# Kernel tuning notes

Measured on AMD Instinct MI355X. Metric: run time of the kernel, lower is better.

Reference implementation:

```python
import jax, jax.numpy as jnp
import numpy as np

B, U, L, H, M = 4, 16, 128, 768, 256   # docs, utterances/doc, tokens/utt, hidden, mentions/doc
HID = 150                               # Score MLP hidden dim
N_CLUSTERS = 32


def setup_inputs() -> dict:
    key = jax.random.key(0)
    ks = jax.random.split(key, 8)
    hidden = jax.random.normal(ks[0], (B, U, L, H), jnp.float32)

    rng = np.random.default_rng(0)
    span_utt = rng.integers(0, U, (B, M))
    span_start = rng.integers(0, L - 8, (B, M))
    span_end = span_start + rng.integers(1, 9, (B, M))  # span length in [1, 8]

    # coreference labels: label[i, j] = 1 iff j is a true antecedent (j < i, same cluster);
    # if mention i has no antecedent, label[i, i] = 1 (the epsilon / new-entity slot).
    clusters = rng.integers(0, N_CLUSTERS, (B, M))
    same = clusters[:, :, None] == clusters[:, None, :]
    ant = same & np.tril(np.ones((M, M), bool), -1)
    labels = ant.astype(np.float32)
    diag = np.arange(M)
    labels[:, diag, diag] = (~ant.any(-1)).astype(np.float32)

    scale = 0.02
    W1 = jax.random.normal(ks[1], (3 * H, HID), jnp.float32) * scale
    W2 = jax.random.normal(ks[2], (HID, HID), jnp.float32) * scale
    W3 = jax.random.normal(ks[3], (HID, 1), jnp.float32) * scale
    return {
        "hidden": hidden,
        "span_utt": jnp.asarray(span_utt, jnp.int32),
        "span_start": jnp.asarray(span_start, jnp.int32),
        "span_end": jnp.asarray(span_end, jnp.int32),
        "labels": jnp.asarray(labels),
        "W1": W1, "b1": jnp.zeros((HID,), jnp.float32),
        "W2": W2, "b2": jnp.zeros((HID,), jnp.float32),
        "W3": W3, "b3": jnp.zeros((1,), jnp.float32),
    }


def reference(hidden, span_utt, span_start, span_end, labels, W1, b1, W2, b2, W3, b3):
    # ---- span mean-pooling (EntityEncoder, aggr='mean') ----
    pos = jnp.arange(L)
    mask = (pos[None, None, :] >= span_start[..., None]) & (pos[None, None, :] < span_end[..., None])
    w = mask.astype(hidden.dtype) / (span_end - span_start)[..., None].astype(hidden.dtype)  # [B,M,L]
    gathered = jnp.take_along_axis(hidden, span_utt[:, :, None, None], axis=1)  # [B,M,L,H]
    pooled = jnp.einsum('bml,bmlh->bmh', w, gathered)  # [B,M,H]

    # ---- pairwise antecedent scoring (PairScorer / Score MLP, dropout=eval) ----
    ii, jj = np.tril_indices(M, -1)  # static pair indices, P = M(M-1)/2
    # concat(i_g, j_g, i_g*j_g) @ W1  ==  i_g@W1a + j_g@W1b + (i_g*j_g)@W1c
    W1a, W1b, W1c = W1[:H], W1[H:2 * H], W1[2 * H:]
    hi = pooled @ W1a   # [B,M,HID]
    hj = pooled @ W1b   # [B,M,HID]
    prod = pooled[:, ii] * pooled[:, jj]                    # [B,P,H]
    h1 = jax.nn.relu(hi[:, ii] + hj[:, jj] + prod @ W1c + b1)
    h2 = jax.nn.relu(h1 @ W2 + b2)
    s = (h2 @ W3 + b3)[..., 0]  # [B,P]

    # ---- per-mention ragged softmax, padded to [M, M] with -1000 ----
    # row i has logits s_ij for j<i plus epsilon=0 at j=i (diagonal of zeros matrix)
    logits = jnp.zeros((B, M, M), hidden.dtype).at[:, ii, jj].set(s)
    valid = jnp.tril(jnp.ones((M, M), bool))
    probs = jax.nn.softmax(jnp.where(valid, logits, -1e30), axis=-1)
    probs = jnp.where(valid, probs, jnp.asarray(-1000.0, hidden.dtype))

    # ---- compute_loss ----
    eps = 1e-8
    prob_sum = jnp.sum(jnp.clip(probs * labels, eps, 1.0 - eps), axis=-1)  # [B,M]
    loss = -jnp.sum(jnp.log(prob_sum))
    return loss
```

## Files before the change

kernel.cpp:

```cpp
#include <hip/hip_runtime.h>
#include <hip/hip_bf16.h>

#define B_ 4
#define U_ 16
#define L_ 128
#define H_ 768
#define M_ 256
#define HID_ 150

typedef _Float16 half8 __attribute__((ext_vector_type(8)));
typedef _Float16 half4t __attribute__((ext_vector_type(4)));
typedef float floatx4 __attribute__((ext_vector_type(4)));

#define MFMA16(af, bf, acc) __builtin_amdgcn_mfma_f32_16x16x32_f16(af, bf, acc, 0, 0, 0)

__global__ __launch_bounds__(256) void prep_pool_kernel(
    const float* __restrict__ W1, const float* __restrict__ W2,
    const float* __restrict__ b2, const float* __restrict__ W3,
    const float* __restrict__ hidden, const int* __restrict__ sutt,
    const int* __restrict__ sstart, const int* __restrict__ send,
    _Float16* __restrict__ W1cs, _Float16* __restrict__ W2s,
    _Float16* __restrict__ W1abs, float2* __restrict__ bw,
    _Float16* __restrict__ pooledh)
{
    if (blockIdx.x >= 1540) {
        const int bm = (blockIdx.x - 1540) * 4 + (threadIdx.x >> 6);
        const int lane = threadIdx.x & 63;
        const int b  = bm >> 8;
        const int u  = sutt[bm];
        const int st = sstart[bm];
        const int en = send[bm];
        const float inv = 1.0f / (float)(en - st);
        const float* src = hidden + ((size_t)(b * U_ + u) * L_) * H_ + lane * 12;
        float4 s[3];
        #pragma unroll
        for (int q = 0; q < 3; ++q) s[q] = make_float4(0.f, 0.f, 0.f, 0.f);
        for (int l = st; l < en; ++l) {
            const float* p = src + (size_t)l * H_;
            #pragma unroll
            for (int q = 0; q < 3; ++q) {
                float4 v = *(const float4*)(p + q * 4);
                s[q].x += v.x; s[q].y += v.y; s[q].z += v.z; s[q].w += v.w;
            }
        }
        _Float16* gp = pooledh + (size_t)bm * H_ + lane * 12;
        #pragma unroll
        for (int q = 0; q < 3; ++q) {
            half4t hv;
            hv[0] = (_Float16)(s[q].x * inv); hv[1] = (_Float16)(s[q].y * inv);
            hv[2] = (_Float16)(s[q].z * inv); hv[3] = (_Float16)(s[q].w * inv);
            *(half4t*)(gp + q * 4) = hv;
        }
        return;
    }
    int idx = blockIdx.x * 256 + threadIdx.x;
    if (blockIdx.x == 0 && threadIdx.x < 160) {
        int n = threadIdx.x;
        bw[n] = (n < HID_) ? make_float2(b2[n], W3[n]) : make_float2(0.f, 0.f);
    }
    if (idx < 122880) {
        int k = idx / 160, n = idx - k * 160;
        float v = (n < HID_) ? W1[(size_t)(2 * H_ + k) * HID_ + n] : 0.f;
        W1cs[((k >> 5) * 10 + (n >> 4)) * 512 +
             (((n & 15) | (((k >> 3) & 3) << 4)) << 3) + (k & 7)] = (_Float16)v;
        return;
    }
    idx -= 122880;
    if (idx < 25600) {
        int k = idx / 160, n = idx - k * 160;
        float v = (k < HID_ && n < HID_) ? W2[(size_t)k * HID_ + n] : 0.f;
        W2s[((k >> 5) * 10 + (n >> 4)) * 512 +
            (((n & 15) | (((k >> 3) & 3) << 4)) << 3) + (k & 7)] = (_Float16)v;
        return;
    }
    idx -= 25600;
    if (idx < 245760) {
        int k = idx / 320, n = idx - k * 320;
        float v = 0.f;
        if (n < HID_) v = W1[(size_t)k * HID_ + n];
        else if (n >= 160 && n < 160 + HID_) v = W1[(size_t)(H_ + k) * HID_ + (n - 160)];
        W1abs[(k >> 5) * 10240 + (n >> 4) * 512 +
              (((n & 15) | (((k >> 3) & 3) << 4)) << 3) + (k & 7)] = (_Float16)v;
    }
}

__global__ __launch_bounds__(64) void hihj_kernel(
    const _Float16* __restrict__ pooledh, const float* __restrict__ b1,
    const _Float16* __restrict__ W1abs,
    float* __restrict__ hiF, float* __restrict__ hjT, float* __restrict__ out)
{
    if (blockIdx.x == 0 && blockIdx.y == 0 && threadIdx.x == 0) *out = 0.f;
    const int rowblk = blockIdx.x;
    const int nq     = blockIdx.y;
    const int lane = threadIdx.x & 63;
    const int g = lane >> 4, l15 = lane & 15;
    floatx4 acc[5];
    #pragma unroll
    for (int u5 = 0; u5 < 5; ++u5) acc[u5] = (floatx4){0.f, 0.f, 0.f, 0.f};
    const _Float16* aB = pooledh + (size_t)(rowblk * 16 + l15) * H_ + g * 8;
    for (int kc = 0; kc < 24; ++kc) {
        half8 av = *(const half8*)(aB + kc * 32);
        #pragma unroll
        for (int u5 = 0; u5 < 5; ++u5) {
            const int u = nq * 5 + u5;
            half8 bv = *(const half8*)(W1abs + (size_t)((kc * 20 + u) * 64 + lane) * 8);
            acc[u5] = MFMA16(av, bv, acc[u5]);
        }
    }
    const int row0 = rowblk * 16 + g * 4;
    #pragma unroll
    for (int u5 = 0; u5 < 5; ++u5) {
        const int n = (nq * 5 + u5) * 16 + l15;
        if (n < HID_) {
            float b1v = b1[n];
            #pragma unroll
            for (int r = 0; r < 4; ++r)
                hiF[(size_t)(row0 + r) * 160 + n] = acc[u5][r] + b1v;
        } else if (n < 160) {
            #pragma unroll
            for (int r = 0; r < 4; ++r)
                hiF[(size_t)(row0 + r) * 160 + n] = 0.f;
        } else if (n < 160 + HID_) {
            *(float4*)&hjT[(size_t)(n - 160) * 1024 + row0] =
                make_float4(acc[u5][0], acc[u5][1], acc[u5][2], acc[u5][3]);
        } else {
            *(float4*)&hjT[(size_t)(n - 160) * 1024 + row0] =
                make_float4(0.f, 0.f, 0.f, 0.f);
        }
    }
}

__global__ __launch_bounds__(256, 2) void pair_mlp_kernel(
    const _Float16* __restrict__ pooledh,
    const float* __restrict__ hiF, const float* __restrict__ hjT,
    const _Float16* __restrict__ W1cs, const _Float16* __restrict__ W2s,
    const float2* __restrict__ bw, const float* __restrict__ b3,
    float* __restrict__ logits)
{
    __shared__ __align__(16) _Float16 smem[26240];
    _Float16* pjL = smem + 21760;

    int q = blockIdx.x;
    const int b = q / 288;
    int r = q - b * 288;
    int h = 0;
    while (r >= 8 * (h + 1)) { r -= 8 * (h + 1); ++h; }
    const int gi = 8 * h + r / (h + 1);
    const int jt = r - (r / (h + 1)) * (h + 1);
    const int i0 = 4 * gi, j0 = 32 * jt;
    const int bm = b * M_;
    const int tid = threadIdx.x;
    const int w = tid >> 6, lane = tid & 63;
    const int g = lane >> 4, l15 = lane & 15;
    const int i = i0 + w;

    floatx4 acc[2][10];
    #pragma unroll
    for (int t = 0; t < 2; ++t)
        #pragma unroll
        for (int u = 0; u < 10; ++u) acc[t][u] = (floatx4){0.f, 0.f, 0.f, 0.f};

    const int prow = tid >> 3, pseg = tid & 7;
    const _Float16* pjg = pooledh + (size_t)(bm + j0 + prow) * H_ + pseg * 8;
    const _Float16* pip = pooledh + (size_t)(bm + i) * H_ + g * 8;

    {
        half8 wst[5];
        #pragma unroll
        for (int q2 = 0; q2 < 5; ++q2)
            wst[q2] = *(const half8*)(W1cs + (size_t)(tid + q2 * 256) * 8);
        half8 pjst = *(const half8*)pjg;
        #pragma unroll
        for (int q2 = 0; q2 < 5; ++q2)
            *(half8*)&smem[(tid + q2 * 256) * 8] = wst[q2];
        *(half8*)&pjL[prow * 70 + pseg * 8] = pjst;
    }
    __syncthreads();

    for (int c = 0; c < 12; ++c) {
        const int cur = c & 1, nxt = cur ^ 1;
        half8 wst[5], pjn;
        if (c < 11) {
            const _Float16* wg = W1cs + (size_t)(c + 1) * 10240;
            #pragma unroll
            for (int q2 = 0; q2 < 5; ++q2)
                wst[q2] = *(const half8*)(wg + (size_t)(tid + q2 * 256) * 8);
            pjn = *(const half8*)(pjg + (c + 1) * 64);
        }
        #pragma unroll
        for (int ks = 0; ks < 2; ++ks) {
            half8 pif = *(const half8*)(pip + c * 64 + ks * 32);
            half8 a0 = *(const half8*)&pjL[cur * 2240 + l15 * 70 + ks * 32 + g * 8] * pif;
            half8 a1 = *(const half8*)&pjL[cur * 2240 + (16 + l15) * 70 + ks * 32 + g * 8] * pif;
            const _Float16* wb = &smem[cur * 10240 + ks * 5120 + lane * 8];
            #pragma unroll
            for (int u = 0; u < 10; ++u) {
                half8 bf = *(const half8*)(wb + u * 512);
                acc[0][u] = MFMA16(a0, bf, acc[0][u]);
                acc[1][u] = MFMA16(a1, bf, acc[1][u]);
            }
        }
        if (c < 11) {
            #pragma unroll
            for (int q2 = 0; q2 < 5; ++q2)
                *(half8*)&smem[nxt * 10240 + (tid + q2 * 256) * 8] = wst[q2];
            *(half8*)&pjL[nxt * 2240 + prow * 70 + pseg * 8] = pjn;
        }
        __syncthreads();
    }

    _Float16* h1w = smem + (size_t)(w * 32) * 170;
    #pragma unroll
    for (int u = 0; u < 10; ++u) {
        const int n = u * 16 + l15;
        float hiv = hiF[(size_t)(bm + i) * 160 + n];
        #pragma unroll
        for (int t = 0; t < 2; ++t) {
            float4 hjv = *(const float4*)&hjT[(size_t)n * 1024 + bm + j0 + t * 16 + g * 4];
            h1w[(t * 16 + g * 4 + 0) * 170 + n] =
                (_Float16)fmaxf(acc[t][u][0] + hiv + hjv.x, 0.f);
            h1w[(t * 16 + g * 4 + 1) * 170 + n] =
                (_Float16)fmaxf(acc[t][u][1] + hiv + hjv.y, 0.f);
            h1w[(t * 16 + g * 4 + 2) * 170 + n] =
                (_Float16)fmaxf(acc[t][u][2] + hiv + hjv.z, 0.f);
            h1w[(t * 16 + g * 4 + 3) * 170 + n] =
                (_Float16)fmaxf(acc[t][u][3] + hiv + hjv.w, 0.f);
        }
    }
    __syncthreads();

    floatx4 acc2[2][10];
    #pragma unroll
    for (int t = 0; t < 2; ++t)
        #pragma unroll
        for (int u = 0; u < 10; ++u) acc2[t][u] = (floatx4){0.f, 0.f, 0.f, 0.f};

    for (int kc2 = 0; kc2 < 5; ++kc2) {
        half8 a20 = *(const half8*)&h1w[(0 * 16 + l15) * 170 + kc2 * 32 + g * 8];
        half8 a21 = *(const half8*)&h1w[(1 * 16 + l15) * 170 + kc2 * 32 + g * 8];
        const _Float16* w2b = W2s + (size_t)kc2 * 5120 + lane * 8;
        #pragma unroll
        for (int u = 0; u < 10; ++u) {
            half8 bf = *(const half8*)(w2b + u * 512);
            acc2[0][u] = MFMA16(a20, bf, acc2[0][u]);
            acc2[1][u] = MFMA16(a21, bf, acc2[1][u]);
        }
    }

    const float b3v = b3[0];
    #pragma unroll
    for (int t = 0; t < 2; ++t) {
        float sr[4] = {0.f, 0.f, 0.f, 0.f};
        #pragma unroll
        for (int u = 0; u < 10; ++u) {
            const int n2 = u * 16 + l15;
            float2 bwv = bw[n2];
            #pragma unroll
            for (int r2 = 0; r2 < 4; ++r2)
                sr[r2] += fmaxf(acc2[t][u][r2] + bwv.x, 0.f) * bwv.y;
        }
        #pragma unroll
        for (int r2 = 0; r2 < 4; ++r2) {
            float s = sr[r2];
            s += __shfl_xor(s, 1);
            s += __shfl_xor(s, 2);
            s += __shfl_xor(s, 4);
            s += __shfl_xor(s, 8);
            if (l15 == 0) {
                const int j = j0 + t * 16 + g * 4 + r2;
                if (j < i)
                    logits[(size_t)(bm + i) * M_ + j] = s + b3v;
            }
        }
    }
}

__global__ __launch_bounds__(256) void loss_kernel(
    const float* __restrict__ logits, const float* __restrict__ labels,
    float* __restrict__ out)
{
    const int bm = blockIdx.x;
    const int i  = bm & (M_ - 1);
    const int j  = threadIdx.x;
    __shared__ float red[4];
    __shared__ float bcast;

    float val = (j < i) ? logits[(size_t)bm * M_ + j]
                        : ((j == i) ? 0.0f : -1e30f);

    float m = val;
    #pragma unroll
    for (int off = 32; off >= 1; off >>= 1) m = fmaxf(m, __shfl_down(m, off, 64));
    const int wave = j >> 6, lane = j & 63;
    if (lane == 0) red[wave] = m;
    __syncthreads();
    if (j == 0) bcast = fmaxf(fmaxf(red[0], red[1]), fmaxf(red[2], red[3]));
    __syncthreads();
    const float mm = bcast;

    float e = (j <= i) ? expf(val - mm) : 0.0f;
    float s = e;
    #pragma unroll
    for (int off = 32; off >= 1; off >>= 1) s += __shfl_down(s, off, 64);
    __syncthreads();
    if (lane == 0) red[wave] = s;
    __syncthreads();
    if (j == 0) bcast = red[0] + red[1] + red[2] + red[3];
    __syncthreads();
    const float ssum = bcast;

    float prob = (j <= i) ? (e / ssum) : -1000.0f;
    float lab = labels[(size_t)bm * M_ + j];
    float tv = prob * lab;
    tv = fminf(fmaxf(tv, 1e-8f), 1.0f - 1e-8f);
    float rs = tv;
    #pragma unroll
    for (int off = 32; off >= 1; off >>= 1) rs += __shfl_down(rs, off, 64);
    __syncthreads();
    if (lane == 0) red[wave] = rs;
    __syncthreads();
    if (j == 0) atomicAdd(out, -logf(red[0] + red[1] + red[2] + red[3]));
}

extern "C" void kernel_launch(void* const* d_in, const int* in_sizes, int n_in,
                              void* d_out, int out_size, void* d_ws, size_t ws_size,
                              hipStream_t stream)
{
    const float* hidden = (const float*)d_in[0];
    const int*   sutt   = (const int*)d_in[1];
    const int*   sstart = (const int*)d_in[2];
    const int*   send   = (const int*)d_in[3];
    const float* labels = (const float*)d_in[4];
    const float* W1     = (const float*)d_in[5];
    const float* b1     = (const float*)d_in[6];
    const float* W2     = (const float*)d_in[7];
    const float* b2     = (const float*)d_in[8];
    const float* W3     = (const float*)d_in[9];
    const float* b3     = (const float*)d_in[10];

    float* ws = (float*)d_ws;
    float*    hiF     = ws;
    float*    hjT     = ws + 163840;
    float*    logits  = ws + 327680;
    float2*   bw      = (float2*)(ws + 589824);
    _Float16* pooledh = (_Float16*)(ws + 590144);
    _Float16* W1cs    = (_Float16*)(ws + 983360);
    _Float16* W2s     = (_Float16*)(ws + 1106240);
    _Float16* W1abs   = (_Float16*)(ws + 1119040);
    float* out = (float*)d_out;

    prep_pool_kernel<<<dim3(1796), 256, 0, stream>>>(
        W1, W2, b2, W3, hidden, sutt, sstart, send,
        W1cs, W2s, W1abs, bw, pooledh);
    hihj_kernel<<<dim3(64, 4), 64, 0, stream>>>(pooledh, b1, W1abs, hiF, hjT, out);
    pair_mlp_kernel<<<dim3(1152), 256, 0, stream>>>(pooledh, hiF, hjT,
                                                    W1cs, W2s, bw, b3, logits);
    loss_kernel<<<dim3(B_ * M_), 256, 0, stream>>>(logits, labels, out);
}
```

Measured before the change: 230.0 us.

## Shrink LDS footprint in pair MLP to fit three blocks per CU

The pair MLP kernel now stages W1c in half-size K chunks (24 steps instead of 12), buffers the pooled-i rows in shared memory instead of reading them from global, and runs the second-layer MLP one 16-row tile at a time so the h1 scratch and acc2 registers halve. Together these cut shared memory per block from about 52KB to about 32KB and reduce register pressure, and the launch bound rises from 2 to 3 blocks per CU for more occupancy. In exchange there are twice as many K-loop barriers and extra syncs between the two layer-2 tiles.

```diff
diff --git a/kernel.cpp b/kernel.cpp
--- a/kernel.cpp
+++ b/kernel.cpp
@@ -130,15 +130,16 @@
     }
 }
 
-__global__ __launch_bounds__(256, 2) void pair_mlp_kernel(
+__global__ __launch_bounds__(256, 3) void pair_mlp_kernel(
     const _Float16* __restrict__ pooledh,
     const float* __restrict__ hiF, const float* __restrict__ hjT,
     const _Float16* __restrict__ W1cs, const _Float16* __restrict__ W2s,
     const float2* __restrict__ bw, const float* __restrict__ b3,
     float* __restrict__ logits)
 {
-    __shared__ __align__(16) _Float16 smem[26240];
-    _Float16* pjL = smem + 21760;
+    __shared__ __align__(16) _Float16 smem[15920];
+    _Float16* pjL = smem + 10880;
+    _Float16* piL = smem + 15360;
 
     int q = blockIdx.x;
     const int b = q / 288;
@@ -162,94 +163,91 @@
 
     const int prow = tid >> 3, pseg = tid & 7;
     const _Float16* pjg = pooledh + (size_t)(bm + j0 + prow) * H_ + pseg * 8;
-    const _Float16* pip = pooledh + (size_t)(bm + i) * H_ + g * 8;
+    const _Float16* pig = pooledh + (size_t)(bm + i0 + (tid >> 3)) * H_ + pseg * 8;
 
     {
-        half8 wst[5];
-        #pragma unroll
-        for (int q2 = 0; q2 < 5; ++q2)
-            wst[q2] = *(const half8*)(W1cs + (size_t)(tid + q2 * 256) * 8);
-        half8 pjst = *(const half8*)pjg;
-        #pragma unroll
-        for (int q2 = 0; q2 < 5; ++q2)
-            *(half8*)&smem[(tid + q2 * 256) * 8] = wst[q2];
-        *(half8*)&pjL[prow * 70 + pseg * 8] = pjst;
-    }
-    __syncthreads();
-
-    for (int c = 0; c < 12; ++c) {
-        const int cur = c & 1, nxt = cur ^ 1;
-        half8 wst[5], pjn;
-        if (c < 11) {
-            const _Float16* wg = W1cs + (size_t)(c + 1) * 10240;
-            #pragma unroll
-            for (int q2 = 0; q2 < 5; ++q2)
-                wst[q2] = *(const half8*)(wg + (size_t)(tid + q2 * 256) * 8);
-            pjn = *(const half8*)(pjg + (c + 1) * 64);
-        }
-        #pragma unroll
-        for (int ks = 0; ks < 2; ++ks) {
-            half8 pif = *(const half8*)(pip + c * 64 + ks * 32);
-            half8 a0 = *(const half8*)&pjL[cur * 2240 + l15 * 70 + ks * 32 + g * 8] * pif;
-            half8 a1 = *(const half8*)&pjL[cur * 2240 + (16 + l15) * 70 + ks * 32 + g * 8] * pif;
-            const _Float16* wb = &smem[cur * 10240 + ks * 5120 + lane * 8];
+        half8 s0 = *(const half8*)(W1cs + (size_t)tid * 8);
+        half8 s1 = *(const half8*)(W1cs + (size_t)(tid + 256) * 8);
+        half8 s2;
+        if (tid < 128) s2 = *(const half8*)(W1cs + (size_t)(tid + 512) * 8);
+        half8 pj0 = *(const half8*)pjg;
+        half8 pi0;
+        if (tid < 32) pi0 = *(const half8*)pig;
+        *(half8*)&smem[tid * 8] = s0;
+        *(half8*)&smem[(tid + 256) * 8] = s1;
+        if (tid < 128) *(half8*)&smem[(tid + 512) * 8] = s2;
+        *(half8*)&pjL[prow * 70 + pseg * 8] = pj0;
+        if (tid < 32) *(half8*)&piL[(tid >> 3) * 70 + pseg * 8] = pi0;
+    }
+    __syncthreads();
+
+    for (int cc = 0; cc < 24; ++cc) {
+        const int wcur = cc & 1, pcur = (cc >> 1) & 1;
+        const bool pfw = (cc < 23);
+        const bool pfp = ((cc & 1) == 0) && (cc < 22);
+        half8 s0, s1, s2, pjn, pin;
+        if (pfw) {
+            const _Float16* wg = W1cs + (size_t)(cc + 1) * 5120;
+            s0 = *(const half8*)(wg + (size_t)tid * 8);
+            s1 = *(const half8*)(wg + (size_t)(tid + 256) * 8);
+            if (tid < 128) s2 = *(const half8*)(wg + (size_t)(tid + 512) * 8);
+        }
+        if (pfp) {
+            pjn = *(const half8*)(pjg + ((cc >> 1) + 1) * 64);
+            if (tid < 32) pin = *(const half8*)(pig + ((cc >> 1) + 1) * 64);
+        }
+        half8 pif = *(const half8*)&piL[pcur * 280 + w * 70 + (cc & 1) * 32 + g * 8];
+        half8 a0 = *(const half8*)&pjL[pcur * 2240 + l15 * 70 + (cc & 1) * 32 + g * 8] * pif;
+        half8 a1 = *(const half8*)&pjL[pcur * 2240 + (16 + l15) * 70 + (cc & 1) * 32 + g * 8] * pif;
+        const _Float16* wb = &smem[wcur * 5120 + lane * 8];
+        #pragma unroll
+        for (int u = 0; u < 10; ++u) {
+            half8 bf = *(const half8*)(wb + u * 512);
+            acc[0][u] = MFMA16(a0, bf, acc[0][u]);
+            acc[1][u] = MFMA16(a1, bf, acc[1][u]);
+        }
+        if (pfw) {
+            _Float16* d = &smem[(wcur ^ 1) * 5120];
+            *(half8*)&d[tid * 8] = s0;
+            *(half8*)&d[(tid + 256) * 8] = s1;
+            if (tid < 128) *(half8*)&d[(tid + 512) * 8] = s2;
+        }
+        if (pfp) {
+            *(half8*)&pjL[(pcur ^ 1) * 2240 + prow * 70 + pseg * 8] = pjn;
+            if (tid < 32) *(half8*)&piL[(pcur ^ 1) * 280 + (tid >> 3) * 70 + pseg * 8] = pin;
+        }
+        __syncthreads();
+    }
+
+    const float b3v = b3[0];
+    _Float16* h1w = smem + (size_t)w * 2720;
+    #pragma unroll
+    for (int lt = 0; lt < 2; ++lt) {
+        #pragma unroll
+        for (int u = 0; u < 10; ++u) {
+            const int n = u * 16 + l15;
+            float hiv = hiF[(size_t)(bm + i) * 160 + n];
+            float4 hjv = *(const float4*)&hjT[(size_t)n * 1024 + bm + j0 + lt * 16 + g * 4];
+            h1w[(g * 4 + 0) * 170 + n] = (_Float16)fmaxf(acc[lt][u][0] + hiv + hjv.x, 0.f);
+            h1w[(g * 4 + 1) * 170 + n] = (_Float16)fmaxf(acc[lt][u][1] + hiv + hjv.y, 0.f);
+            h1w[(g * 4 + 2) * 170 + n] = (_Float16)fmaxf(acc[lt][u][2] + hiv + hjv.z, 0.f);
+            h1w[(g * 4 + 3) * 170 + n] = (_Float16)fmaxf(acc[lt][u][3] + hiv + hjv.w, 0.f);
+        }
+        __syncthreads();
+
+        floatx4 acc2[10];
+        #pragma unroll
+        for (int u = 0; u < 10; ++u) acc2[u] = (floatx4){0.f, 0.f, 0.f, 0.f};
+        for (int kc2 = 0; kc2 < 5; ++kc2) {
+            half8 a2 = *(const half8*)&h1w[l15 * 170 + kc2 * 32 + g * 8];
+            const _Float16* w2b = W2s + (size_t)kc2 * 5120 + lane * 8;
             #pragma unroll
             for (int u = 0; u < 10; ++u) {
-                half8 bf = *(const half8*)(wb + u * 512);
-                acc[0][u] = MFMA16(a0, bf, acc[0][u]);
-                acc[1][u] = MFMA16(a1, bf, acc[1][u]);
+                half8 bf = *(const half8*)(w2b + u * 512);
+                acc2[u] = MFMA16(a2, bf, acc2[u]);
             }
         }
-        if (c < 11) {
-            #pragma unroll
-            for (int q2 = 0; q2 < 5; ++q2)
-                *(half8*)&smem[nxt * 10240 + (tid + q2 * 256) * 8] = wst[q2];
-            *(half8*)&pjL[nxt * 2240 + prow * 70 + pseg * 8] = pjn;
-        }
-        __syncthreads();
-    }
-
-    _Float16* h1w = smem + (size_t)(w * 32) * 170;
-    #pragma unroll
-    for (int u = 0; u < 10; ++u) {
-        const int n = u * 16 + l15;
-        float hiv = hiF[(size_t)(bm + i) * 160 + n];
-        #pragma unroll
-        for (int t = 0; t < 2; ++t) {
-            float4 hjv = *(const float4*)&hjT[(size_t)n * 1024 + bm + j0 + t * 16 + g * 4];
-            h1w[(t * 16 + g * 4 + 0) * 170 + n] =
-                (_Float16)fmaxf(acc[t][u][0] + hiv + hjv.x, 0.f);
-            h1w[(t * 16 + g * 4 + 1) * 170 + n] =
-                (_Float16)fmaxf(acc[t][u][1] + hiv + hjv.y, 0.f);
-            h1w[(t * 16 + g * 4 + 2) * 170 + n] =
-                (_Float16)fmaxf(acc[t][u][2] + hiv + hjv.z, 0.f);
-            h1w[(t * 16 + g * 4 + 3) * 170 + n] =
-                (_Float16)fmaxf(acc[t][u][3] + hiv + hjv.w, 0.f);
-        }
-    }
-    __syncthreads();
-
-    floatx4 acc2[2][10];
-    #pragma unroll
-    for (int t = 0; t < 2; ++t)
-        #pragma unroll
-        for (int u = 0; u < 10; ++u) acc2[t][u] = (floatx4){0.f, 0.f, 0.f, 0.f};
-
-    for (int kc2 = 0; kc2 < 5; ++kc2) {
-        half8 a20 = *(const half8*)&h1w[(0 * 16 + l15) * 170 + kc2 * 32 + g * 8];
-        half8 a21 = *(const half8*)&h1w[(1 * 16 + l15) * 170 + kc2 * 32 + g * 8];
-        const _Float16* w2b = W2s + (size_t)kc2 * 5120 + lane * 8;
-        #pragma unroll
-        for (int u = 0; u < 10; ++u) {
-            half8 bf = *(const half8*)(w2b + u * 512);
-            acc2[0][u] = MFMA16(a20, bf, acc2[0][u]);
-            acc2[1][u] = MFMA16(a21, bf, acc2[1][u]);
-        }
-    }
-
-    const float b3v = b3[0];
-    #pragma unroll
-    for (int t = 0; t < 2; ++t) {
+
         float sr[4] = {0.f, 0.f, 0.f, 0.f};
         #pragma unroll
         for (int u = 0; u < 10; ++u) {
@@ -257,7 +255,7 @@
             float2 bwv = bw[n2];
             #pragma unroll
             for (int r2 = 0; r2 < 4; ++r2)
-                sr[r2] += fmaxf(acc2[t][u][r2] + bwv.x, 0.f) * bwv.y;
+                sr[r2] += fmaxf(acc2[u][r2] + bwv.x, 0.f) * bwv.y;
         }
         #pragma unroll
         for (int r2 = 0; r2 < 4; ++r2) {
@@ -267,11 +265,12 @@
             s += __shfl_xor(s, 4);
             s += __shfl_xor(s, 8);
             if (l15 == 0) {
-                const int j = j0 + t * 16 + g * 4 + r2;
+                const int j = j0 + lt * 16 + g * 4 + r2;
                 if (j < i)
                     logits[(size_t)(bm + i) * M_ + j] = s + b3v;
             }
         }
+        __syncthreads();
     }
 }
 
```

Measured after the change: 247.1 us. 1.07x slower.
